# Optimization experiments

Hardware: AMD Instinct MI355X
Metric: run time of the kernel (lower is better)

Reference implementation:

```python
import jax, jax.numpy as jnp
import numpy as np

DIM = 2048
N_HEADS = 16
N_KV_HEADS = 4
HEAD_DIM = DIM // N_HEADS  # 128
T = 2048


def setup_inputs() -> dict:
    key = jax.random.key(0)
    k1, k2, k3 = jax.random.split(key, 3)
    scale = 1.0 / np.sqrt(DIM)
    x = jax.random.normal(k1, (T, DIM), dtype=jnp.float32)
    # GQA-consistent fused QKV projection: q (n_h*hd) + k (n_kv*hd) + v (n_kv*hd)
    qkv_out = (N_HEADS + 2 * N_KV_HEADS) * HEAD_DIM  # 3072
    W_qkv = jax.random.normal(k2, (DIM, qkv_out), dtype=jnp.float32) * scale
    W_o = jax.random.normal(k3, (N_HEADS * HEAD_DIM, DIM), dtype=jnp.float32) * scale
    return {"x": x, "W_qkv": W_qkv, "W_o": W_o}


def reference(x, W_qkv, W_o):
    Tn, C = x.shape
    hd = HEAD_DIM
    qkv = x @ W_qkv  # [T, (n_h + 2*n_kv)*hd]
    q, k, v = jnp.split(qkv, [N_HEADS * hd, (N_HEADS + N_KV_HEADS) * hd], axis=-1)
    q = q.reshape(Tn, N_HEADS, hd).transpose(1, 0, 2)      # [n_h, T, hd]
    k = k.reshape(Tn, N_KV_HEADS, hd).transpose(1, 0, 2)   # [n_kv, T, hd]
    v = v.reshape(Tn, N_KV_HEADS, hd).transpose(1, 0, 2)
    rep = N_HEADS // N_KV_HEADS
    k = jnp.repeat(k, rep, axis=0)  # [n_h, T, hd]
    v = jnp.repeat(v, rep, axis=0)
    scores = jnp.einsum('hid,hjd->hij', q, k) / jnp.sqrt(jnp.asarray(hd, x.dtype))
    causal = jnp.tril(jnp.ones((Tn, Tn), dtype=bool))[None, :, :]
    scores = jnp.where(causal, scores, -jnp.inf)
    attn = jax.nn.softmax(scores, axis=-1)
    out = jnp.einsum('hij,hjd->hid', attn, v)  # [n_h, T, hd]
    out = out.transpose(1, 0, 2).reshape(Tn, N_HEADS * hd)
    return out @ W_o
```

## Files before the change

### kernel.cpp

```cpp
#include <hip/hip_runtime.h>
#include <stdint.h>

#define T_SEQ   2048
#define DMODEL  2048
#define NH      16
#define HD      128
#define QKVN    3072
#define KCOL    2048
#define VCOL    2560

typedef __bf16 bf16x8 __attribute__((ext_vector_type(8)));
typedef float  f32x4  __attribute__((ext_vector_type(4)));
typedef unsigned short u16x8 __attribute__((ext_vector_type(8)));

__device__ __forceinline__ uint16_t f2bf(float f) {
    uint32_t u = __builtin_bit_cast(uint32_t, f);
    u += 0x7fffu + ((u >> 16) & 1u);
    return (uint16_t)(u >> 16);
}
__device__ __forceinline__ float bf2f(uint16_t u) {
    return __builtin_bit_cast(float, (uint32_t)u << 16);
}
__device__ __forceinline__ u16x8 ld8(const uint16_t* p) {
    return *reinterpret_cast<const u16x8*>(p);
}
__device__ __forceinline__ void st8(uint16_t* p, u16x8 v) {
    *reinterpret_cast<u16x8*>(p) = v;
}
__device__ __forceinline__ bf16x8 as_bf(u16x8 v) { return __builtin_bit_cast(bf16x8, v); }

__device__ __forceinline__ void gl_lds16(const uint16_t* g, uint16_t* l) {
    __builtin_amdgcn_global_load_lds((const __attribute__((address_space(1))) void*)g,
                                     (__attribute__((address_space(3))) void*)l, 16, 0, 0);
}

__global__ __launch_bounds__(256) void k_cast(const float* __restrict__ in,
                                              uint16_t* __restrict__ out, int n8) {
    int i = blockIdx.x * 256 + threadIdx.x;
    if (i >= n8) return;
    const f32x4* p = reinterpret_cast<const f32x4*>(in) + (size_t)i * 2;
    f32x4 a = p[0], b = p[1];
    u16x8 o;
    o[0] = f2bf(a[0]); o[1] = f2bf(a[1]); o[2] = f2bf(a[2]); o[3] = f2bf(a[3]);
    o[4] = f2bf(b[0]); o[5] = f2bf(b[1]); o[6] = f2bf(b[2]); o[7] = f2bf(b[3]);
    reinterpret_cast<u16x8*>(out)[i] = o;
}

__global__ __launch_bounds__(256) void k_tcast(const float* __restrict__ in,
                                               uint16_t* __restrict__ out, int R, int C) {
    __shared__ uint16_t tile[64][72];
    int t = threadIdx.x;
    int rbase = blockIdx.y * 64, cbase = blockIdx.x * 64;
#pragma unroll
    for (int p = 0; p < 4; ++p) {
        int ir = p * 16 + (t >> 4);
        int ic = (t & 15) * 4;
        f32x4 v = *reinterpret_cast<const f32x4*>(&in[(size_t)(rbase + ir) * C + cbase + ic]);
        tile[ir][ic + 0] = f2bf(v[0]);
        tile[ir][ic + 1] = f2bf(v[1]);
        tile[ir][ic + 2] = f2bf(v[2]);
        tile[ir][ic + 3] = f2bf(v[3]);
    }
    __syncthreads();
#pragma unroll
    for (int p = 0; p < 2; ++p) {
        int oc = p * 32 + (t >> 3);
        int orr = (t & 7) * 8;
        u16x8 o;
#pragma unroll
        for (int e = 0; e < 8; ++e) o[e] = tile[orr + e][oc];
        st8(&out[(size_t)(cbase + oc) * R + rbase + orr], o);
    }
}

__global__ __launch_bounds__(256) void k_tbf16(const uint16_t* __restrict__ in,
                                               uint16_t* __restrict__ out,
                                               int R, int C, int ldin, int coff) {
    __shared__ uint16_t tile[64][72];
    int t = threadIdx.x;
    int rbase = blockIdx.y * 64, cbase = blockIdx.x * 64;
#pragma unroll
    for (int p = 0; p < 2; ++p) {
        int ir = p * 32 + (t >> 3);
        int ic = (t & 7) * 8;
        u16x8 v = ld8(&in[(size_t)(rbase + ir) * ldin + coff + cbase + ic]);
#pragma unroll
        for (int e = 0; e < 8; ++e) tile[ir][ic + e] = v[e];
    }
    __syncthreads();
#pragma unroll
    for (int p = 0; p < 2; ++p) {
        int oc = p * 32 + (t >> 3);
        int orr = (t & 7) * 8;
        u16x8 o;
#pragma unroll
        for (int e = 0; e < 8; ++e) o[e] = tile[orr + e][oc];
        st8(&out[(size_t)(cbase + oc) * R + rbase + orr], o);
    }
}

__global__ __launch_bounds__(256) void k_gemm(const uint16_t* __restrict__ A,
                                              const uint16_t* __restrict__ Bt,
                                              void* __restrict__ Cout,
                                              int M, int N, int K, int gy,
                                              int out_bf16, int scale_cols, float qscale) {
    __shared__ __align__(16) uint16_t Asm[2][64 * 32];
    __shared__ __align__(16) uint16_t Bsm[2][128 * 32];
    int t = threadIdx.x;
    int w = t >> 6, lane = t & 63, lo = lane & 15, g4 = lane >> 4;

    int nwg = (int)gridDim.x;
    int wg = (int)blockIdx.x;
    int idx = (wg & 7) * (nwg >> 3) + (wg >> 3);
    int bx = idx / gy, by = idx % gy;
    int mbase = by * 64, nbase = bx * 128;

    int wm = w >> 1, wn = w & 1;

    int srowA = w * 16 + (lane >> 2);
    int scol = (lane & 3) * 8;
    const uint16_t* pA = A + (size_t)(mbase + srowA) * K + scol;
    int srowB0 = w * 32 + (lane >> 2);
    int srowB1 = srowB0 + 16;
    const uint16_t* pB0 = Bt + (size_t)(nbase + srowB0) * K + scol;
    const uint16_t* pB1 = Bt + (size_t)(nbase + srowB1) * K + scol;
    int lofsA = w * 512, lofsB0 = w * 1024, lofsB1 = lofsB0 + 512;

    f32x4 acc[2][4] = {};

    gl_lds16(pA, &Asm[0][lofsA]);
    gl_lds16(pB0, &Bsm[0][lofsB0]); gl_lds16(pB1, &Bsm[0][lofsB1]);

    int cur = 0;
    for (int kt = 0; kt < K; kt += 32) {
        __syncthreads();
        if (kt + 32 < K) {
            int ko = kt + 32;
            gl_lds16(pA + ko, &Asm[cur ^ 1][lofsA]);
            gl_lds16(pB0 + ko, &Bsm[cur ^ 1][lofsB0]); gl_lds16(pB1 + ko, &Bsm[cur ^ 1][lofsB1]);
        }
        bf16x8 af[2], bfr[4];
#pragma unroll
        for (int i = 0; i < 2; ++i) {
            int ar = wm * 32 + i * 16 + lo;
            af[i] = as_bf(ld8(&Asm[cur][ar * 32 + g4 * 8]));
        }
#pragma unroll
        for (int j = 0; j < 4; ++j) {
            int br = wn * 64 + j * 16 + lo;
            bfr[j] = as_bf(ld8(&Bsm[cur][br * 32 + g4 * 8]));
        }
        __builtin_amdgcn_s_setprio(1);
#pragma unroll
        for (int i = 0; i < 2; ++i)
#pragma unroll
            for (int j = 0; j < 4; ++j)
                acc[i][j] = __builtin_amdgcn_mfma_f32_16x16x32_bf16(af[i], bfr[j], acc[i][j], 0, 0, 0);
        __builtin_amdgcn_s_setprio(0);
        cur ^= 1;
    }

    if (out_bf16) {
        uint16_t* C = (uint16_t*)Cout;
#pragma unroll
        for (int i = 0; i < 2; ++i)
#pragma unroll
            for (int j = 0; j < 4; ++j)
#pragma unroll
                for (int r = 0; r < 4; ++r) {
                    int row = mbase + wm * 32 + i * 16 + g4 * 4 + r;
                    int col = nbase + wn * 64 + j * 16 + lo;
                    float v = acc[i][j][r];
                    if (col < scale_cols) v *= qscale;
                    C[(size_t)row * N + col] = f2bf(v);
                }
    } else {
        float* C = (float*)Cout;
#pragma unroll
        for (int i = 0; i < 2; ++i)
#pragma unroll
            for (int j = 0; j < 4; ++j)
#pragma unroll
                for (int r = 0; r < 4; ++r) {
                    int row = mbase + wm * 32 + i * 16 + g4 * 4 + r;
                    int col = nbase + wn * 64 + j * 16 + lo;
                    C[(size_t)row * N + col] = acc[i][j][r];
                }
    }
}

__global__ __launch_bounds__(256) void k_attn(const uint16_t* __restrict__ qkv,
                                              const uint16_t* __restrict__ vt,
                                              uint16_t* __restrict__ po,
                                              float* __restrict__ pml) {
    __shared__ __align__(16) uint16_t Ksm[2][64 * 128];
    __shared__ __align__(16) uint16_t Vsm[2][128 * 64];
    __shared__ __align__(16) uint16_t Psm[4][16 * 64];
    int t = threadIdx.x;
    int w = t >> 6, lane = t & 63, lo = lane & 15, g4 = lane >> 4;
    int x = blockIdx.x, h = blockIdx.y, p = blockIdx.z, kh = h >> 2;

    const uint16_t* kbase = qkv + KCOL + (size_t)kh * HD;
    const uint16_t* vbase = vt + (size_t)(kh * HD) * T_SEQ;

    const uint16_t* kp[4]; const uint16_t* vp[4]; int lofs[4];
#pragma unroll
    for (int c = 0; c < 4; ++c) {
        int ch = w * 4 + c;
        int kr = ch * 4 + (lane >> 4);
        kp[c] = kbase + (size_t)kr * QKVN + ((lane & 15) ^ (kr & 7)) * 8;
        int vr = ch * 8 + (lane >> 3);
        vp[c] = vbase + (size_t)vr * T_SEQ + ((lane & 7) ^ (vr & 7)) * 8;
        lofs[c] = ch * 512;
    }

    for (int rep = 0; rep < 2; ++rep) {
        int qt = rep ? 31 - x : x;
        int qb = qt * 64;
        int cnt = (qt + 2 - p) >> 1;

        bf16x8 qf[4];
        {
            int qrow = qb + w * 16 + lo;
            const uint16_t* qp = &qkv[(size_t)qrow * QKVN + h * HD + g4 * 8];
#pragma unroll
            for (int ks = 0; ks < 4; ++ks) qf[ks] = as_bf(ld8(qp + ks * 32));
        }

        f32x4 o[8] = {};
        float mr[4], pp[4];
#pragma unroll
        for (int r = 0; r < 4; ++r) { mr[r] = -INFINITY; pp[r] = 0.f; }

        if (cnt) {
            __syncthreads();
            size_t ko = (size_t)p * 64 * QKVN; int vo = p * 64;
#pragma unroll
            for (int c = 0; c < 4; ++c) {
                gl_lds16(kp[c] + ko, &Ksm[0][lofs[c]]);
                gl_lds16(vp[c] + vo, &Vsm[0][lofs[c]]);
            }
        }

        int cur = 0;
        for (int it = 0; it < cnt; ++it) {
            int jt = p + 2 * it;
            __syncthreads();
            if (it + 1 < cnt) {
                size_t ko = (size_t)(jt + 2) * 64 * QKVN;
                int vo = (jt + 2) * 64;
#pragma unroll
                for (int c = 0; c < 4; ++c) {
                    gl_lds16(kp[c] + ko, &Ksm[cur ^ 1][lofs[c]]);
                    gl_lds16(vp[c] + vo, &Vsm[cur ^ 1][lofs[c]]);
                }
            }

            f32x4 s[4] = {};
            __builtin_amdgcn_s_setprio(1);
#pragma unroll
            for (int nt = 0; nt < 4; ++nt) {
                int j = nt * 16 + lo;
#pragma unroll
                for (int ks = 0; ks < 4; ++ks) {
                    bf16x8 b = as_bf(ld8(&Ksm[cur][(j * 128 + ks * 32 + g4 * 8) ^ ((lo & 7) << 3)]));
                    s[nt] = __builtin_amdgcn_mfma_f32_16x16x32_bf16(qf[ks], b, s[nt], 0, 0, 0);
                }
            }
            __builtin_amdgcn_s_setprio(0);

            if (jt == qt) {
#pragma unroll
                for (int nt = 0; nt < 4; ++nt)
#pragma unroll
                    for (int r = 0; r < 4; ++r) {
                        int j = nt * 16 + lo;
                        int i = w * 16 + g4 * 4 + r;
                        if (j > i) s[nt][r] = -INFINITY;
                    }
            }

            float pm[4];
#pragma unroll
            for (int r = 0; r < 4; ++r) {
                pm[r] = fmaxf(fmaxf(s[0][r], s[1][r]), fmaxf(s[2][r], s[3][r]));
                pm[r] = fmaxf(pm[r], __shfl_xor(pm[r], 1));
                pm[r] = fmaxf(pm[r], __shfl_xor(pm[r], 2));
                pm[r] = fmaxf(pm[r], __shfl_xor(pm[r], 4));
                pm[r] = fmaxf(pm[r], __shfl_xor(pm[r], 8));
            }
            bool grow = false;
#pragma unroll
            for (int r = 0; r < 4; ++r) grow = grow || (pm[r] > mr[r] + 8.f);
            if (__any(grow)) {
#pragma unroll
                for (int r = 0; r < 4; ++r) {
                    float mn = fmaxf(mr[r], pm[r]);
                    float al = __expf(mr[r] - mn);
                    mr[r] = mn;
                    pp[r] *= al;
#pragma unroll
                    for (int dt = 0; dt < 8; ++dt) o[dt][r] *= al;
                }
            }
#pragma unroll
            for (int nt = 0; nt < 4; ++nt)
#pragma unroll
                for (int r = 0; r < 4; ++r) {
                    float pe = __expf(s[nt][r] - mr[r]);
                    s[nt][r] = pe;
                    pp[r] += pe;
                }
#pragma unroll
            for (int nt = 0; nt < 4; ++nt)
#pragma unroll
                for (int r = 0; r < 4; ++r) {
                    int i = g4 * 4 + r, j = nt * 16 + lo;
                    Psm[w][(i * 64 + j) ^ ((i & 7) << 3)] = f2bf(s[nt][r]);
                }

            __builtin_amdgcn_s_setprio(1);
#pragma unroll
            for (int ks2 = 0; ks2 < 2; ++ks2) {
                bf16x8 pa = as_bf(ld8(&Psm[w][(lo * 64 + ks2 * 32 + g4 * 8) ^ ((lo & 7) << 3)]));
#pragma unroll
                for (int dt = 0; dt < 8; ++dt) {
                    int d = dt * 16 + lo;
                    bf16x8 vb = as_bf(ld8(&Vsm[cur][(d * 64 + ks2 * 32 + g4 * 8) ^ ((lo & 7) << 3)]));
                    o[dt] = __builtin_amdgcn_mfma_f32_16x16x32_bf16(pa, vb, o[dt], 0, 0, 0);
                }
            }
            __builtin_amdgcn_s_setprio(0);
            cur ^= 1;
        }

        float lr[4];
#pragma unroll
        for (int r = 0; r < 4; ++r) {
            float ps = pp[r];
            ps += __shfl_xor(ps, 1);
            ps += __shfl_xor(ps, 2);
            ps += __shfl_xor(ps, 4);
            ps += __shfl_xor(ps, 8);
            lr[r] = ps;
        }

        uint16_t* pob = po + (size_t)p * T_SEQ * DMODEL;
#pragma unroll
        for (int dt = 0; dt < 8; ++dt)
#pragma unroll
            for (int r = 0; r < 4; ++r) {
                int i = qb + w * 16 + g4 * 4 + r;
                int col = h * HD + dt * 16 + lo;
                pob[(size_t)i * DMODEL + col] = f2bf(o[dt][r]);
            }
        if (lo == 0) {
#pragma unroll
            for (int r = 0; r < 4; ++r) {
                int i = qb + w * 16 + g4 * 4 + r;
                float* pe = pml + ((size_t)(p * T_SEQ + i) * NH + h) * 2;
                pe[0] = mr[r];
                pe[1] = lr[r];
            }
        }
    }
}

__global__ __launch_bounds__(256) void k_comb(const uint16_t* __restrict__ po,
                                              const float* __restrict__ pml,
                                              uint16_t* __restrict__ ao) {
    int i = blockIdx.x * 256 + threadIdx.x;
    int row = i >> 8;
    int cg = i & 255;
    int h = cg >> 4;
    int col = cg * 8;
    const float* p0 = pml + ((size_t)row * NH + h) * 2;
    const float* p1 = pml + ((size_t)(T_SEQ + row) * NH + h) * 2;
    float m0 = p0[0], l0 = p0[1], m1 = p1[0], l1 = p1[1];
    float m = fmaxf(m0, m1);
    float w0 = __expf(m0 - m), w1 = __expf(m1 - m);
    float rl = 1.f / (l0 * w0 + l1 * w1);
    size_t off = (size_t)row * DMODEL + col;
    u16x8 a = ld8(po + off);
    u16x8 b = ld8(po + (size_t)T_SEQ * DMODEL + off);
    u16x8 o;
#pragma unroll
    for (int e = 0; e < 8; ++e)
        o[e] = f2bf((bf2f(a[e]) * w0 + bf2f(b[e]) * w1) * rl);
    st8(ao + off, o);
}

extern "C" void kernel_launch(void* const* d_in, const int* in_sizes, int n_in,
                              void* d_out, int out_size, void* d_ws, size_t ws_size,
                              hipStream_t stream) {
    (void)in_sizes; (void)n_in; (void)out_size; (void)ws_size;
    const float* x    = (const float*)d_in[0];
    const float* Wqkv = (const float*)d_in[1];
    const float* Wo   = (const float*)d_in[2];
    float* out = (float*)d_out;

    char* ws = (char*)d_ws;
    uint16_t* xb   = (uint16_t*)(ws + 0);
    uint16_t* wqt  = (uint16_t*)(ws + 8388608);
    uint16_t* wot  = (uint16_t*)(ws + 20971520);
    uint16_t* qkvb = (uint16_t*)(ws + 29360128);
    uint16_t* vtb  = (uint16_t*)(ws + 41943040);
    uint16_t* aob  = (uint16_t*)(ws + 44040192);
    uint16_t* po   = (uint16_t*)(ws + 0);
    float*    pml  = (float*)(ws + 16777216);

    const float qscale = 0.08838834764831845f;

    k_cast<<<2048, 256, 0, stream>>>(x, xb, 524288);
    k_tcast<<<dim3(48, 32), 256, 0, stream>>>(Wqkv, wqt, 2048, 3072);
    k_tcast<<<dim3(32, 32), 256, 0, stream>>>(Wo, wot, 2048, 2048);
    k_gemm<<<768, 256, 0, stream>>>(xb, wqt, qkvb, 2048, 3072, 2048, 32, 1, 2048, qscale);
    k_tbf16<<<dim3(8, 32), 256, 0, stream>>>(qkvb, vtb, 2048, 512, 3072, 2560);
    k_attn<<<dim3(16, 16, 2), 256, 0, stream>>>(qkvb, vtb, po, pml);
    k_comb<<<2048, 256, 0, stream>>>(po, pml, aob);
    k_gemm<<<512, 256, 0, stream>>>(aob, wot, out, 2048, 2048, 2048, 32, 0, 0, 1.0f);
}
```

Measured before the change: 151.3 us.

## Deepen GEMM K-tile with swizzled LDS and restructure attention into 3-way KV split

The GEMM now stages 64-wide K tiles with an XOR-swizzled LDS layout, halving the number of barrier-separated iterations and reducing bank conflicts. Attention moves to 32-key tiles with a 3-way KV split across the grid z dimension. It computes the transposed score (K as the A operand) so each lane owns one query row, which removes most shuffles for the row max and sum. Softmax uses exp2 with log2e folded into the q scale, a packed bf16 convert for P, and a larger rescale threshold. The combine kernel merges three partials in place, reusing the workspace so the output projection reads directly from it. These changes add more partial traffic and smaller MFMA work per tile, in exchange for finer load balance and fewer reductions.

```diff
diff --git a/kernel.cpp b/kernel.cpp
--- a/kernel.cpp
+++ b/kernel.cpp
@@ -28,6 +28,12 @@
     *reinterpret_cast<u16x8*>(p) = v;
 }
 __device__ __forceinline__ bf16x8 as_bf(u16x8 v) { return __builtin_bit_cast(bf16x8, v); }
+
+__device__ __forceinline__ uint32_t cvtpk(float a, float b) {
+    uint32_t r;
+    asm("v_cvt_pk_bf16_f32 %0, %1, %2" : "=v"(r) : "v"(a), "v"(b));
+    return r;
+}
 
 __device__ __forceinline__ void gl_lds16(const uint16_t* g, uint16_t* l) {
     __builtin_amdgcn_global_load_lds((const __attribute__((address_space(1))) void*)g,
@@ -104,8 +110,8 @@
                                               void* __restrict__ Cout,
                                               int M, int N, int K, int gy,
                                               int out_bf16, int scale_cols, float qscale) {
-    __shared__ __align__(16) uint16_t Asm[2][64 * 32];
-    __shared__ __align__(16) uint16_t Bsm[2][128 * 32];
+    __shared__ __align__(16) uint16_t Asm[2][64 * 64];
+    __shared__ __align__(16) uint16_t Bsm[2][128 * 64];
     int t = threadIdx.x;
     int w = t >> 6, lane = t & 63, lo = lane & 15, g4 = lane >> 4;
 
@@ -117,45 +123,62 @@
 
     int wm = w >> 1, wn = w & 1;
 
-    int srowA = w * 16 + (lane >> 2);
-    int scol = (lane & 3) * 8;
-    const uint16_t* pA = A + (size_t)(mbase + srowA) * K + scol;
-    int srowB0 = w * 32 + (lane >> 2);
-    int srowB1 = srowB0 + 16;
-    const uint16_t* pB0 = Bt + (size_t)(nbase + srowB0) * K + scol;
-    const uint16_t* pB1 = Bt + (size_t)(nbase + srowB1) * K + scol;
-    int lofsA = w * 512, lofsB0 = w * 1024, lofsB1 = lofsB0 + 512;
+    const uint16_t* pA[2]; int lofsA[2];
+#pragma unroll
+    for (int c = 0; c < 2; ++c) {
+        int ch = w * 2 + c;
+        int r = ch * 8 + (lane >> 3);
+        pA[c] = A + (size_t)(mbase + r) * K + (((lane & 7) ^ (r & 7)) * 8);
+        lofsA[c] = ch * 512;
+    }
+    const uint16_t* pB[4]; int lofsB[4];
+#pragma unroll
+    for (int c = 0; c < 4; ++c) {
+        int ch = w * 4 + c;
+        int r = ch * 8 + (lane >> 3);
+        pB[c] = Bt + (size_t)(nbase + r) * K + (((lane & 7) ^ (r & 7)) * 8);
+        lofsB[c] = ch * 512;
+    }
 
     f32x4 acc[2][4] = {};
 
-    gl_lds16(pA, &Asm[0][lofsA]);
-    gl_lds16(pB0, &Bsm[0][lofsB0]); gl_lds16(pB1, &Bsm[0][lofsB1]);
+#pragma unroll
+    for (int c = 0; c < 2; ++c) gl_lds16(pA[c], &Asm[0][lofsA[c]]);
+#pragma unroll
+    for (int c = 0; c < 4; ++c) gl_lds16(pB[c], &Bsm[0][lofsB[c]]);
 
     int cur = 0;
-    for (int kt = 0; kt < K; kt += 32) {
+    for (int kt = 0; kt < K; kt += 64) {
         __syncthreads();
-        if (kt + 32 < K) {
-            int ko = kt + 32;
-            gl_lds16(pA + ko, &Asm[cur ^ 1][lofsA]);
-            gl_lds16(pB0 + ko, &Bsm[cur ^ 1][lofsB0]); gl_lds16(pB1 + ko, &Bsm[cur ^ 1][lofsB1]);
-        }
-        bf16x8 af[2], bfr[4];
-#pragma unroll
-        for (int i = 0; i < 2; ++i) {
-            int ar = wm * 32 + i * 16 + lo;
-            af[i] = as_bf(ld8(&Asm[cur][ar * 32 + g4 * 8]));
-        }
-#pragma unroll
-        for (int j = 0; j < 4; ++j) {
-            int br = wn * 64 + j * 16 + lo;
-            bfr[j] = as_bf(ld8(&Bsm[cur][br * 32 + g4 * 8]));
+        if (kt + 64 < K) {
+            int ko = kt + 64;
+#pragma unroll
+            for (int c = 0; c < 2; ++c) gl_lds16(pA[c] + ko, &Asm[cur ^ 1][lofsA[c]]);
+#pragma unroll
+            for (int c = 0; c < 4; ++c) gl_lds16(pB[c] + ko, &Bsm[cur ^ 1][lofsB[c]]);
+        }
+        bf16x8 af[2][2], bfr[2][4];
+#pragma unroll
+        for (int ks = 0; ks < 2; ++ks) {
+#pragma unroll
+            for (int i = 0; i < 2; ++i) {
+                int ar = wm * 32 + i * 16 + lo;
+                af[ks][i] = as_bf(ld8(&Asm[cur][(ar * 64 + ks * 32 + g4 * 8) ^ ((lo & 7) << 3)]));
+            }
+#pragma unroll
+            for (int j = 0; j < 4; ++j) {
+                int br = wn * 64 + j * 16 + lo;
+                bfr[ks][j] = as_bf(ld8(&Bsm[cur][(br * 64 + ks * 32 + g4 * 8) ^ ((lo & 7) << 3)]));
+            }
         }
         __builtin_amdgcn_s_setprio(1);
 #pragma unroll
-        for (int i = 0; i < 2; ++i)
-#pragma unroll
-            for (int j = 0; j < 4; ++j)
-                acc[i][j] = __builtin_amdgcn_mfma_f32_16x16x32_bf16(af[i], bfr[j], acc[i][j], 0, 0, 0);
+        for (int ks = 0; ks < 2; ++ks)
+#pragma unroll
+            for (int i = 0; i < 2; ++i)
+#pragma unroll
+                for (int j = 0; j < 4; ++j)
+                    acc[i][j] = __builtin_amdgcn_mfma_f32_16x16x32_bf16(af[ks][i], bfr[ks][j], acc[i][j], 0, 0, 0);
         __builtin_amdgcn_s_setprio(0);
         cur ^= 1;
     }
@@ -193,31 +216,31 @@
                                               const uint16_t* __restrict__ vt,
                                               uint16_t* __restrict__ po,
                                               float* __restrict__ pml) {
-    __shared__ __align__(16) uint16_t Ksm[2][64 * 128];
-    __shared__ __align__(16) uint16_t Vsm[2][128 * 64];
-    __shared__ __align__(16) uint16_t Psm[4][16 * 64];
+    __shared__ __align__(16) uint16_t Ksm[2][32 * 128];
+    __shared__ __align__(16) uint16_t Vsm[2][128 * 32];
+    __shared__ __align__(16) uint16_t Psm[4][16 * 40];
     int t = threadIdx.x;
     int w = t >> 6, lane = t & 63, lo = lane & 15, g4 = lane >> 4;
-    int x = blockIdx.x, h = blockIdx.y, p = blockIdx.z, kh = h >> 2;
+    int x = blockIdx.x, h = blockIdx.y, sp = blockIdx.z, kh = h >> 2;
 
     const uint16_t* kbase = qkv + KCOL + (size_t)kh * HD;
     const uint16_t* vbase = vt + (size_t)(kh * HD) * T_SEQ;
 
-    const uint16_t* kp[4]; const uint16_t* vp[4]; int lofs[4];
-#pragma unroll
-    for (int c = 0; c < 4; ++c) {
-        int ch = w * 4 + c;
+    const uint16_t* kp[2]; const uint16_t* vp[2]; int lofs[2];
+#pragma unroll
+    for (int c = 0; c < 2; ++c) {
+        int ch = w * 2 + c;
         int kr = ch * 4 + (lane >> 4);
         kp[c] = kbase + (size_t)kr * QKVN + ((lane & 15) ^ (kr & 7)) * 8;
-        int vr = ch * 8 + (lane >> 3);
-        vp[c] = vbase + (size_t)vr * T_SEQ + ((lane & 7) ^ (vr & 7)) * 8;
+        int vr = ch * 16 + (lane >> 2);
+        vp[c] = vbase + (size_t)vr * T_SEQ + (lane & 3) * 8;
         lofs[c] = ch * 512;
     }
 
     for (int rep = 0; rep < 2; ++rep) {
         int qt = rep ? 31 - x : x;
         int qb = qt * 64;
-        int cnt = (qt + 2 - p) >> 1;
+        int cnt = (2 * qt + 4 - sp) / 3;
 
         bf16x8 qf[4];
         {
@@ -228,15 +251,13 @@
         }
 
         f32x4 o[8] = {};
-        float mr[4], pp[4];
-#pragma unroll
-        for (int r = 0; r < 4; ++r) { mr[r] = -INFINITY; pp[r] = 0.f; }
+        float mr = -INFINITY, pp = 0.f;
 
         if (cnt) {
             __syncthreads();
-            size_t ko = (size_t)p * 64 * QKVN; int vo = p * 64;
-#pragma unroll
-            for (int c = 0; c < 4; ++c) {
+            size_t ko = (size_t)sp * 32 * QKVN; int vo = sp * 32;
+#pragma unroll
+            for (int c = 0; c < 2; ++c) {
                 gl_lds16(kp[c] + ko, &Ksm[0][lofs[c]]);
                 gl_lds16(vp[c] + vo, &Vsm[0][lofs[c]]);
             }
@@ -244,108 +265,97 @@
 
         int cur = 0;
         for (int it = 0; it < cnt; ++it) {
-            int jt = p + 2 * it;
+            int jt = sp + 3 * it;
             __syncthreads();
             if (it + 1 < cnt) {
-                size_t ko = (size_t)(jt + 2) * 64 * QKVN;
-                int vo = (jt + 2) * 64;
-#pragma unroll
-                for (int c = 0; c < 4; ++c) {
+                size_t ko = (size_t)(jt + 3) * 32 * QKVN;
+                int vo = (jt + 3) * 32;
+#pragma unroll
+                for (int c = 0; c < 2; ++c) {
                     gl_lds16(kp[c] + ko, &Ksm[cur ^ 1][lofs[c]]);
                     gl_lds16(vp[c] + vo, &Vsm[cur ^ 1][lofs[c]]);
                 }
             }
 
-            f32x4 s[4] = {};
+            f32x4 s[2] = {};
             __builtin_amdgcn_s_setprio(1);
 #pragma unroll
-            for (int nt = 0; nt < 4; ++nt) {
+            for (int nt = 0; nt < 2; ++nt) {
                 int j = nt * 16 + lo;
 #pragma unroll
                 for (int ks = 0; ks < 4; ++ks) {
-                    bf16x8 b = as_bf(ld8(&Ksm[cur][(j * 128 + ks * 32 + g4 * 8) ^ ((lo & 7) << 3)]));
-                    s[nt] = __builtin_amdgcn_mfma_f32_16x16x32_bf16(qf[ks], b, s[nt], 0, 0, 0);
+                    bf16x8 a = as_bf(ld8(&Ksm[cur][(j * 128 + ks * 32 + g4 * 8) ^ ((lo & 7) << 3)]));
+                    s[nt] = __builtin_amdgcn_mfma_f32_16x16x32_bf16(a, qf[ks], s[nt], 0, 0, 0);
                 }
             }
             __builtin_amdgcn_s_setprio(0);
 
-            if (jt == qt) {
-#pragma unroll
-                for (int nt = 0; nt < 4; ++nt)
+            if (jt >= 2 * qt) {
+                int jb = jt * 32;
+                int i = qb + w * 16 + lo;
+#pragma unroll
+                for (int nt = 0; nt < 2; ++nt)
 #pragma unroll
                     for (int r = 0; r < 4; ++r) {
-                        int j = nt * 16 + lo;
-                        int i = w * 16 + g4 * 4 + r;
+                        int j = jb + nt * 16 + g4 * 4 + r;
                         if (j > i) s[nt][r] = -INFINITY;
                     }
             }
 
-            float pm[4];
-#pragma unroll
-            for (int r = 0; r < 4; ++r) {
-                pm[r] = fmaxf(fmaxf(s[0][r], s[1][r]), fmaxf(s[2][r], s[3][r]));
-                pm[r] = fmaxf(pm[r], __shfl_xor(pm[r], 1));
-                pm[r] = fmaxf(pm[r], __shfl_xor(pm[r], 2));
-                pm[r] = fmaxf(pm[r], __shfl_xor(pm[r], 4));
-                pm[r] = fmaxf(pm[r], __shfl_xor(pm[r], 8));
-            }
-            bool grow = false;
-#pragma unroll
-            for (int r = 0; r < 4; ++r) grow = grow || (pm[r] > mr[r] + 8.f);
-            if (__any(grow)) {
+            float pm = fmaxf(fmaxf(fmaxf(s[0][0], s[0][1]), fmaxf(s[0][2], s[0][3])),
+                             fmaxf(fmaxf(s[1][0], s[1][1]), fmaxf(s[1][2], s[1][3])));
+            pm = fmaxf(pm, __shfl_xor(pm, 16));
+            pm = fmaxf(pm, __shfl_xor(pm, 32));
+
+            if (__any(pm > mr + 11.f)) {
+                float mn = fmaxf(mr, pm);
+                float msafe_old = fmaxf(mr, -1e30f);
+                float al = exp2f(fminf(msafe_old - mn, 0.f));
+                mr = mn;
+                pp *= al;
+                float alo[4];
+#pragma unroll
+                for (int r = 0; r < 4; ++r)
+                    alo[r] = __shfl(al, (lane & 48) | (((lane >> 4) << 2) + r));
+#pragma unroll
+                for (int dt = 0; dt < 8; ++dt)
+#pragma unroll
+                    for (int r = 0; r < 4; ++r) o[dt][r] *= alo[r];
+            }
+            float msafe = fmaxf(mr, -1e30f);
+#pragma unroll
+            for (int nt = 0; nt < 2; ++nt)
 #pragma unroll
                 for (int r = 0; r < 4; ++r) {
-                    float mn = fmaxf(mr[r], pm[r]);
-                    float al = __expf(mr[r] - mn);
-                    mr[r] = mn;
-                    pp[r] *= al;
-#pragma unroll
-                    for (int dt = 0; dt < 8; ++dt) o[dt][r] *= al;
+                    float pe = exp2f(s[nt][r] - msafe);
+                    s[nt][r] = pe;
+                    pp += pe;
                 }
-            }
-#pragma unroll
-            for (int nt = 0; nt < 4; ++nt)
-#pragma unroll
-                for (int r = 0; r < 4; ++r) {
-                    float pe = __expf(s[nt][r] - mr[r]);
-                    s[nt][r] = pe;
-                    pp[r] += pe;
-                }
-#pragma unroll
-            for (int nt = 0; nt < 4; ++nt)
-#pragma unroll
-                for (int r = 0; r < 4; ++r) {
-                    int i = g4 * 4 + r, j = nt * 16 + lo;
-                    Psm[w][(i * 64 + j) ^ ((i & 7) << 3)] = f2bf(s[nt][r]);
-                }
-
+#pragma unroll
+            for (int nt = 0; nt < 2; ++nt) {
+                uint32_t p01 = cvtpk(s[nt][0], s[nt][1]);
+                uint32_t p23 = cvtpk(s[nt][2], s[nt][3]);
+                *reinterpret_cast<uint2*>(&Psm[w][lo * 40 + nt * 16 + g4 * 4]) =
+                    make_uint2(p01, p23);
+            }
+
+            bf16x8 pa = as_bf(ld8(&Psm[w][lo * 40 + g4 * 8]));
             __builtin_amdgcn_s_setprio(1);
 #pragma unroll
-            for (int ks2 = 0; ks2 < 2; ++ks2) {
-                bf16x8 pa = as_bf(ld8(&Psm[w][(lo * 64 + ks2 * 32 + g4 * 8) ^ ((lo & 7) << 3)]));
-#pragma unroll
-                for (int dt = 0; dt < 8; ++dt) {
-                    int d = dt * 16 + lo;
-                    bf16x8 vb = as_bf(ld8(&Vsm[cur][(d * 64 + ks2 * 32 + g4 * 8) ^ ((lo & 7) << 3)]));
-                    o[dt] = __builtin_amdgcn_mfma_f32_16x16x32_bf16(pa, vb, o[dt], 0, 0, 0);
-                }
+            for (int dt = 0; dt < 8; ++dt) {
+                int d = dt * 16 + lo;
+                bf16x8 vb = as_bf(ld8(&Vsm[cur][d * 32 + g4 * 8]));
+                o[dt] = __builtin_amdgcn_mfma_f32_16x16x32_bf16(pa, vb, o[dt], 0, 0, 0);
             }
             __builtin_amdgcn_s_setprio(0);
             cur ^= 1;
         }
 
-        float lr[4];
-#pragma unroll
-        for (int r = 0; r < 4; ++r) {
-            float ps = pp[r];
-            ps += __shfl_xor(ps, 1);
-            ps += __shfl_xor(ps, 2);
-            ps += __shfl_xor(ps, 4);
-            ps += __shfl_xor(ps, 8);
-            lr[r] = ps;
-        }
-
-        uint16_t* pob = po + (size_t)p * T_SEQ * DMODEL;
+        float lr = pp;
+        lr += __shfl_xor(lr, 16);
+        lr += __shfl_xor(lr, 32);
+
+        uint16_t* pob = po + (size_t)sp * T_SEQ * DMODEL;
 #pragma unroll
         for (int dt = 0; dt < 8; ++dt)
 #pragma unroll
@@ -354,40 +364,40 @@
                 int col = h * HD + dt * 16 + lo;
                 pob[(size_t)i * DMODEL + col] = f2bf(o[dt][r]);
             }
-        if (lo == 0) {
-#pragma unroll
-            for (int r = 0; r < 4; ++r) {
-                int i = qb + w * 16 + g4 * 4 + r;
-                float* pe = pml + ((size_t)(p * T_SEQ + i) * NH + h) * 2;
-                pe[0] = mr[r];
-                pe[1] = lr[r];
-            }
-        }
-    }
-}
-
-__global__ __launch_bounds__(256) void k_comb(const uint16_t* __restrict__ po,
-                                              const float* __restrict__ pml,
-                                              uint16_t* __restrict__ ao) {
+        if (lane < 16) {
+            int i = qb + w * 16 + lane;
+            float* pe = pml + (size_t)sp * T_SEQ * NH * 2 + ((size_t)i * NH + h) * 2;
+            pe[0] = mr;
+            pe[1] = lr;
+        }
+    }
+}
+
+__global__ __launch_bounds__(256) void k_comb(uint16_t* __restrict__ po,
+                                              const float* __restrict__ pml) {
     int i = blockIdx.x * 256 + threadIdx.x;
     int row = i >> 8;
     int cg = i & 255;
     int h = cg >> 4;
     int col = cg * 8;
-    const float* p0 = pml + ((size_t)row * NH + h) * 2;
-    const float* p1 = pml + ((size_t)(T_SEQ + row) * NH + h) * 2;
-    float m0 = p0[0], l0 = p0[1], m1 = p1[0], l1 = p1[1];
-    float m = fmaxf(m0, m1);
-    float w0 = __expf(m0 - m), w1 = __expf(m1 - m);
-    float rl = 1.f / (l0 * w0 + l1 * w1);
+    const size_t PS = (size_t)T_SEQ * NH * 2;
+    const size_t TD = (size_t)T_SEQ * DMODEL;
+    size_t mo = ((size_t)row * NH + h) * 2;
+    float m0 = pml[mo], l0 = pml[mo + 1];
+    float m1 = pml[PS + mo], l1 = pml[PS + mo + 1];
+    float m2 = pml[2 * PS + mo], l2 = pml[2 * PS + mo + 1];
+    float m = fmaxf(fmaxf(m0, m1), m2);
+    float w0 = exp2f(m0 - m), w1 = exp2f(m1 - m), w2 = exp2f(m2 - m);
+    float rl = 1.f / (l0 * w0 + l1 * w1 + l2 * w2);
     size_t off = (size_t)row * DMODEL + col;
     u16x8 a = ld8(po + off);
-    u16x8 b = ld8(po + (size_t)T_SEQ * DMODEL + off);
+    u16x8 b = ld8(po + TD + off);
+    u16x8 c = ld8(po + 2 * TD + off);
     u16x8 o;
 #pragma unroll
     for (int e = 0; e < 8; ++e)
-        o[e] = f2bf((bf2f(a[e]) * w0 + bf2f(b[e]) * w1) * rl);
-    st8(ao + off, o);
+        o[e] = f2bf((bf2f(a[e]) * w0 + bf2f(b[e]) * w1 + bf2f(c[e]) * w2) * rl);
+    st8(po + off, o);
 }
 
 extern "C" void kernel_launch(void* const* d_in, const int* in_sizes, int n_in,
@@ -402,21 +412,20 @@
     char* ws = (char*)d_ws;
     uint16_t* xb   = (uint16_t*)(ws + 0);
     uint16_t* wqt  = (uint16_t*)(ws + 8388608);
-    uint16_t* wot  = (uint16_t*)(ws + 20971520);
-    uint16_t* qkvb = (uint16_t*)(ws + 29360128);
-    uint16_t* vtb  = (uint16_t*)(ws + 41943040);
-    uint16_t* aob  = (uint16_t*)(ws + 44040192);
     uint16_t* po   = (uint16_t*)(ws + 0);
-    float*    pml  = (float*)(ws + 16777216);
-
-    const float qscale = 0.08838834764831845f;
+    float*    pml  = (float*)(ws + 25165824);
+    uint16_t* wot  = (uint16_t*)(ws + 25952256);
+    uint16_t* qkvb = (uint16_t*)(ws + 34340864);
+    uint16_t* vtb  = (uint16_t*)(ws + 46923776);
+
+    const float qscale = 0.12751743f;
 
     k_cast<<<2048, 256, 0, stream>>>(x, xb, 524288);
     k_tcast<<<dim3(48, 32), 256, 0, stream>>>(Wqkv, wqt, 2048, 3072);
     k_tcast<<<dim3(32, 32), 256, 0, stream>>>(Wo, wot, 2048, 2048);
     k_gemm<<<768, 256, 0, stream>>>(xb, wqt, qkvb, 2048, 3072, 2048, 32, 1, 2048, qscale);
     k_tbf16<<<dim3(8, 32), 256, 0, stream>>>(qkvb, vtb, 2048, 512, 3072, 2560);
-    k_attn<<<dim3(16, 16, 2), 256, 0, stream>>>(qkvb, vtb, po, pml);
-    k_comb<<<2048, 256, 0, stream>>>(po, pml, aob);
-    k_gemm<<<512, 256, 0, stream>>>(aob, wot, out, 2048, 2048, 2048, 32, 0, 0, 1.0f);
-}
+    k_attn<<<dim3(16, 16, 3), 256, 0, stream>>>(qkvb, vtb, po, pml);
+    k_comb<<<2048, 256, 0, stream>>>(po, pml);
+    k_gemm<<<512, 256, 0, stream>>>(po, wot, out, 2048, 2048, 2048, 32, 0, 0, 1.0f);
+}
```

New measurement: 155.8 us. +3.0%, slower.
